# Performance work log

Hardware: AMD Instinct MI355X
Metric: run time of the kernel (lower is better)

The kernel has to match this reference:

```python
import jax, jax.numpy as jnp
import numpy as np

T, B, IN, H, OUT = 1024, 128, 6, 1536, 5


def setup_inputs() -> dict:
    key = jax.random.key(0)
    ks = jax.random.split(key, 11)
    s = 1.0 / np.sqrt(H)  # PyTorch cell init range
    u = lambda k, shape: jax.random.uniform(k, shape, jnp.float32, -s, s)
    return {
        "rnn_input": jax.random.normal(ks[0], (T, B, IN), jnp.float32),
        "W_ih0": u(ks[1], (4 * H, IN)),
        "W_hh0": u(ks[2], (4 * H, H)),
        "b_ih0": u(ks[3], (4 * H,)),
        "b_hh0": u(ks[4], (4 * H,)),
        "W_ih1": u(ks[5], (4 * H, H)),
        "W_hh1": u(ks[6], (4 * H, H)),
        "b_ih1": u(ks[7], (4 * H,)),
        "b_hh1": u(ks[8], (4 * H,)),
        "W_lin": u(ks[9], (OUT, H)),
        "b_lin": u(ks[10], (OUT,)),
    }


def _lstm_cell(x, h, c, W_ih, W_hh, b):
    # PyTorch LSTMCell: gates ordered (input, forget, cell, output)
    gates = x @ W_ih.T + h @ W_hh.T + b  # [B, 4H]
    i, f, g, o = jnp.split(gates, 4, axis=-1)
    c_new = jax.nn.sigmoid(f) * c + jax.nn.sigmoid(i) * jnp.tanh(g)
    h_new = jax.nn.sigmoid(o) * jnp.tanh(c_new)
    return h_new, c_new


def reference(rnn_input, W_ih0, W_hh0, b_ih0, b_hh0,
              W_ih1, W_hh1, b_ih1, b_hh1, W_lin, b_lin):
    b0 = b_ih0 + b_hh0
    b1 = b_ih1 + b_hh1
    batch = rnn_input.shape[1]
    h = rnn_input.dtype
    z = jnp.zeros((batch, H), h)

    def step(carry, x_t):
        h0, c0, h1, c1 = carry
        h0, c0 = _lstm_cell(x_t, h0, c0, W_ih0, W_hh0, b0)
        h1, c1 = _lstm_cell(h0, h1, c1, W_ih1, W_hh1, b1)
        return (h0, c0, h1, c1), None

    (h0, c0, h1, c1), _ = jax.lax.scan(step, (z, z, z, z), rnn_input)
    # Module's forward returns only the last-timestep linear output
    return h1 @ W_lin.T + b_lin  # [B, OUT]
```

## Files before the change

kernel.cpp:

```cpp
#include <hip/hip_runtime.h>

#define TSTEPS 1024
#define BATCH  128
#define HDIM   1536
#define NB_L0  96
#define NB_L1  128
#define NBLK   (NB_L0 + NB_L1)
#define K0P    1600
#define K1P    3072

typedef _Float16 f16x8 __attribute__((ext_vector_type(8)));
typedef float    f32x4 __attribute__((ext_vector_type(4)));

#define OFF_C0   0ul
#define OFF_C1   1024ul
#define OFF_H0   4096ul
#define OFF_H1   (OFF_H0 + 4ul*BATCH*HDIM*2)
#define OFF_WP0  (OFF_H1 + 2ul*BATCH*HDIM*2)
#define OFF_WP1  (OFF_WP0 + 96ul*64*K0P*2)
#define OFF_WLP  (OFF_WP1 + 128ul*48*K1P*2)
#define WS_NEED  (OFF_WLP + 16ul*HDIM*2)

#define SM_PARK  98304
#define SM_CST   147456
#define SM_BG    155648
#define SM_BYTES 155904

#define MFMA(a,b,c) __builtin_amdgcn_mfma_f32_16x16x32_f16(a,b,c,0,0,0)
#define LDSBAR()  asm volatile("s_waitcnt lgkmcnt(0)\n\ts_barrier" ::: "memory")
#define WAITVM8() asm volatile("s_waitcnt vmcnt(8)" ::: "memory")
#define WAITVM0() asm volatile("s_waitcnt vmcnt(0)" ::: "memory")

__device__ __forceinline__ float sgf(float x) { return 1.f/(1.f + __expf(-x)); }
__device__ __forceinline__ float thf(float x) { float e = __expf(2.f*x); return 1.f - 2.f/(e+1.f); }

__device__ __forceinline__ void gld16(const _Float16* g, char* lds) {
  __builtin_amdgcn_global_load_lds(
      (const __attribute__((address_space(1))) unsigned int*)g,
      (__attribute__((address_space(3))) unsigned int*)lds, 16, 0, 0);
}

__device__ __forceinline__ void group_bar(unsigned* lines, unsigned target, int tid) {
  __syncthreads();
  if (tid == 0)
    __hip_atomic_fetch_add(lines + (blockIdx.x & 7)*32, 1u,
                           __ATOMIC_RELEASE, __HIP_MEMORY_SCOPE_AGENT);
  if (tid < 8) {
    while (__hip_atomic_load(lines + tid*32, __ATOMIC_RELAXED,
                             __HIP_MEMORY_SCOPE_AGENT) < target)
      __builtin_amdgcn_s_sleep(1);
    __builtin_amdgcn_fence(__ATOMIC_ACQUIRE, "agent");
  }
  __syncthreads();
}

__device__ __forceinline__ void wait_group(unsigned* lines, unsigned target, int tid) {
  if (tid < 8) {
    while (__hip_atomic_load(lines + tid*32, __ATOMIC_RELAXED,
                             __HIP_MEMORY_SCOPE_AGENT) < target)
      __builtin_amdgcn_s_sleep(1);
    __builtin_amdgcn_fence(__ATOMIC_ACQUIRE, "agent");
  }
  __syncthreads();
}

__global__ void convert_weights(const float* __restrict__ Wih0, const float* __restrict__ Whh0,
                                const float* __restrict__ Wih1, const float* __restrict__ Whh1,
                                const float* __restrict__ Wlin,
                                _Float16* __restrict__ Wp0, _Float16* __restrict__ Wp1,
                                _Float16* __restrict__ Wlp) {
  const unsigned N0 = 96u*64u*K0P, N1 = 128u*48u*K1P, N2 = 16u*HDIM;
  const unsigned NT = N0 + N1 + N2;
  for (unsigned i = blockIdx.x*blockDim.x + threadIdx.x; i < NT; i += gridDim.x*blockDim.x) {
    if (i < N0) {
      unsigned blk = i / (64u*K0P), r = i - blk*64u*K0P;
      unsigned p = r / K0P, kk = r - p*K0P;
      unsigned srow = (p>>4)*HDIM + blk*16 + (p&15);
      float v;
      if (kk < 64u) v = (kk < 6u) ? Wih0[srow*6 + kk] : 0.f;
      else          v = Whh0[(size_t)srow*HDIM + (kk-64u)];
      Wp0[i] = (_Float16)v;
    } else if (i < N0 + N1) {
      unsigned ii = i - N0;
      unsigned blk = ii / (48u*K1P), r = ii - blk*48u*K1P;
      unsigned p = r / K1P, kk = r - p*K1P;
      unsigned srow = (p/12u)*HDIM + blk*12 + (p%12u);
      float v = (kk < (unsigned)HDIM) ? Wih1[(size_t)srow*HDIM + kk]
                                      : Whh1[(size_t)srow*HDIM + (kk-HDIM)];
      Wp1[ii] = (_Float16)v;
    } else {
      unsigned ii = i - N0 - N1;
      unsigned rr = ii / HDIM, k = ii - rr*HDIM;
      Wlp[ii] = (_Float16)(rr < 5 ? Wlin[rr*HDIM + k] : 0.f);
    }
  }
}

__global__ __launch_bounds__(256, 1) void lstm_persistent(
    const float* __restrict__ xall,
    const float* __restrict__ bih0, const float* __restrict__ bhh0,
    const float* __restrict__ bih1, const float* __restrict__ bhh1,
    const float* __restrict__ blin,
    const _Float16* __restrict__ Wp0, const _Float16* __restrict__ Wp1,
    const _Float16* __restrict__ Wlp,
    _Float16* __restrict__ h0b, _Float16* __restrict__ h1b,
    unsigned* __restrict__ c0l, unsigned* __restrict__ c1l,
    float* __restrict__ out)
{
  extern __shared__ __align__(16) char smem[];
  char*  park = smem + SM_PARK;
  float* cst  = (float*)(smem + SM_CST);
  float* bg   = (float*)(smem + SM_BG);
  float* gbuf = (float*)smem;

  const int tid = threadIdx.x, bid = blockIdx.x;
  const int wv = tid >> 6, lane = tid & 63, q = lane >> 4, l15 = lane & 15;
  const int BH = BATCH*HDIM;

  int dmaoff[8];
#pragma unroll
  for (int i = 0; i < 8; ++i) {
    int m = wv*32 + i*4 + (lane>>4), w16 = lane & 15;
    int u = (w16 & 8) | ((w16 ^ (m & 7)) & 7);
    dmaoff[i] = m*HDIM + u*8;
  }
  const int uA = wv*4 + q;
  int addrA[8];
#pragma unroll
  for (int mt = 0; mt < 8; ++mt) {
    int m = mt*16 + l15;
    int swz = (uA & 8) | ((uA ^ (m & 7)) & 7);
    addrA[mt] = m*256 + swz*16;
  }

  if (bid < NB_L0) {
    for (int p = tid; p < 64; p += 256) {
      int srow = (p>>4)*HDIM + (bid<<4) + (p&15);
      bg[p] = bih0[srow] + bhh0[srow];
    }
    for (int i = tid; i < BATCH*16; i += 256) cst[i] = 0.f;
    f16x8 bw[13][4];
#pragma unroll
    for (int wi = 0; wi < 13; ++wi)
#pragma unroll
      for (int nt = 0; nt < 4; ++nt)
        bw[wi][nt] = *(const f16x8*)(Wp0 + ((size_t)(bid*64 + nt*16 + l15))*K0P
                                         + (4*wi + wv)*32 + q*8);
    __syncthreads();

#pragma unroll 1
    for (int s = 0; s < TSTEPS; ++s) {
      if (s >= 4) wait_group(c1l, 16u*(unsigned)(s-3), tid);

      const _Float16* h0r = h0b + (size_t)((s+3)&3)*BH;
      _Float16*       h0w = h0b + (size_t)(s&3)*BH;
      const float*    xs  = xall + (size_t)s*BATCH*6;

#pragma unroll
      for (int i = 0; i < 8; ++i)
        gld16(h0r + 64 + dmaoff[i], smem + 32768 + (wv*8+i)*1024);
#pragma unroll
      for (int i = 0; i < 4; ++i) {
        int sidx = i*256 + tid, m = sidx>>3, w8 = sidx&7;
        int u = w8 ^ (m & 7);
        f16x8 v = {0,0,0,0,0,0,0,0};
        if (u == 0) {
#pragma unroll
          for (int j = 0; j < 6; ++j) v[j] = (_Float16)xs[m*6 + j];
        }
        *(f16x8*)(smem + m*256 + w8*16) = v;
      }
#pragma unroll
      for (int i = 0; i < 4; ++i) {
        int sidx = i*256 + tid, m = sidx>>3, w8 = sidx&7;
        int u8 = (w8 ^ (m & 7)) & 7;
        f16x8 hv = *(const f16x8*)(h0r + m*HDIM + u8*8);
        *(f16x8*)(smem + m*256 + (8 + w8)*16) = hv;
      }
      f32x4 acc[8][4];
#pragma unroll
      for (int mt = 0; mt < 8; ++mt)
#pragma unroll
        for (int nt = 0; nt < 4; ++nt) { f32x4 z = {0,0,0,0}; acc[mt][nt] = z; }

#pragma unroll
      for (int wi = 0; wi < 13; ++wi) {
        if (wi == 12)      WAITVM0();
        else if (wi >= 1)  WAITVM8();
        LDSBAR();
        if (wi + 2 < 13) {
          const _Float16* src = h0r + (wi+2)*128 - 64;
          char* dst = smem + ((wi+2)%3)*32768;
#pragma unroll
          for (int i = 0; i < 8; ++i) gld16(src + dmaoff[i], dst + (wv*8+i)*1024);
        }
        if (4*wi + wv < 50) {
          const char* bs = smem + (wi%3)*32768;
#pragma unroll
          for (int mt = 0; mt < 8; ++mt) {
            f16x8 a = *(const f16x8*)(bs + addrA[mt]);
#pragma unroll
            for (int nt = 0; nt < 4; ++nt)
              acc[mt][nt] = MFMA(a, bw[wi][nt], acc[mt][nt]);
          }
        }
      }
      LDSBAR();

#pragma unroll
      for (int r = 0; r < 4; ++r) {
        int nt = (wv + r) & 3;
#pragma unroll
        for (int mt = 0; mt < 8; ++mt) {
          f32x4 av = (nt==0)?acc[mt][0]:(nt==1)?acc[mt][1]:(nt==2)?acc[mt][2]:acc[mt][3];
          float* p = gbuf + (nt*16 + l15)*132 + (mt*16 + q*4);
          if (r == 0) *(f32x4*)p = av;
          else        { f32x4 o = *(const f32x4*)p; *(f32x4*)p = o + av; }
        }
        LDSBAR();
      }
#pragma unroll
      for (int e = 0; e < 8; ++e) {
        int idx = e*256 + tid, m = idx>>4, j = idx&15;
        float gi = gbuf[j*132 + m]        + bg[j];
        float gf = gbuf[(16+j)*132 + m]   + bg[16+j];
        float gg = gbuf[(32+j)*132 + m]   + bg[32+j];
        float go = gbuf[(48+j)*132 + m]   + bg[48+j];
        float co = cst[m*16 + j];
        float cn = sgf(gf)*co + sgf(gi)*thf(gg);
        cst[m*16 + j] = cn;
        h0w[(size_t)m*HDIM + (bid<<4) + j] = (_Float16)(sgf(go)*thf(cn));
      }
      group_bar(c0l, 12u*(unsigned)(s+1), tid);
    }
  } else {
    const int bid1 = bid - NB_L0;
    for (int p = tid; p < 48; p += 256) {
      int srow = (p/12)*HDIM + bid1*12 + (p%12);
      bg[p] = bih1[srow] + bhh1[srow];
    }
    for (int i = tid; i < 64*12; i += 256) cst[i] = 0.f;
    f16x8 bw1[20][3];
#pragma unroll
    for (int wi = 0; wi < 20; ++wi)
#pragma unroll
      for (int nt = 0; nt < 3; ++nt)
        bw1[wi][nt] = *(const f16x8*)(Wp1 + ((size_t)(bid1*48 + nt*16 + l15))*K1P
                                          + (4*wi + wv)*32 + q*8);
    for (int idx = tid; idx < 16*3*64; idx += 256) {
      int cl = idx/192, rem = idx - cl*192, nt = rem>>6, l = rem&63;
      f16x8 v = *(const f16x8*)(Wp1 + ((size_t)(bid1*48 + nt*16 + (l&15)))*K1P
                                    + (80 + cl)*32 + (l>>4)*8);
      *(f16x8*)(park + idx*16) = v;
    }
    __syncthreads();

#pragma unroll 1
    for (int s = 1; s <= TSTEPS; ++s) {
      wait_group(c0l, 12u*(unsigned)s, tid);

      const _Float16* h0r = h0b + (size_t)((s-1)&3)*BH;
      const _Float16* h1r = h1b + (size_t)(s&1)*BH;
      _Float16*       h1w = h1b + (size_t)((s-1)&1)*BH;

#pragma unroll
      for (int i = 0; i < 8; ++i) gld16(h0r +   0 + dmaoff[i], smem +     0 + (wv*8+i)*1024);
#pragma unroll
      for (int i = 0; i < 8; ++i) gld16(h0r + 128 + dmaoff[i], smem + 32768 + (wv*8+i)*1024);
      f32x4 acc[8][3];
#pragma unroll
      for (int mt = 0; mt < 8; ++mt)
#pragma unroll
        for (int nt = 0; nt < 3; ++nt) { f32x4 z = {0,0,0,0}; acc[mt][nt] = z; }

#pragma unroll
      for (int wi = 0; wi < 24; ++wi) {
        if (wi == 23) WAITVM0(); else WAITVM8();
        LDSBAR();
        if (wi + 2 < 24) {
          int wn = wi + 2;
          const _Float16* src = (wn < 12) ? (h0r + wn*128) : (h1r + (wn-12)*128);
          char* dst = smem + (wn%3)*32768;
#pragma unroll
          for (int i = 0; i < 8; ++i) gld16(src + dmaoff[i], dst + (wv*8+i)*1024);
        }
        const char* bs = smem + (wi%3)*32768;
        if (wi < 20) {
#pragma unroll
          for (int mt = 0; mt < 8; ++mt) {
            f16x8 a = *(const f16x8*)(bs + addrA[mt]);
#pragma unroll
            for (int nt = 0; nt < 3; ++nt)
              acc[mt][nt] = MFMA(a, bw1[wi][nt], acc[mt][nt]);
          }
        } else {
          f16x8 p0 = *(const f16x8*)(park + ((((wi-20)*4 + wv)*3 + 0)*64 + lane)*16);
          f16x8 p1 = *(const f16x8*)(park + ((((wi-20)*4 + wv)*3 + 1)*64 + lane)*16);
          f16x8 p2 = *(const f16x8*)(park + ((((wi-20)*4 + wv)*3 + 2)*64 + lane)*16);
#pragma unroll
          for (int mt = 0; mt < 8; ++mt) {
            f16x8 a = *(const f16x8*)(bs + addrA[mt]);
            acc[mt][0] = MFMA(a, p0, acc[mt][0]);
            acc[mt][1] = MFMA(a, p1, acc[mt][1]);
            acc[mt][2] = MFMA(a, p2, acc[mt][2]);
          }
        }
      }
      LDSBAR();

#pragma unroll
      for (int r = 0; r < 4; ++r) {
        int nt = (wv + r) & 3;
        if (nt < 3) {
#pragma unroll
          for (int mt = 0; mt < 8; ++mt) {
            f32x4 av = (nt==0)?acc[mt][0]:(nt==1)?acc[mt][1]:acc[mt][2];
            float* p = gbuf + (nt*16 + l15)*132 + (mt*16 + q*4);
            if (r == 0) *(f32x4*)p = av;
            else        { f32x4 o = *(const f32x4*)p; *(f32x4*)p = o + av; }
          }
        }
        LDSBAR();
      }
#pragma unroll
      for (int e = 0; e < 8; ++e) {
        int idx = e*256 + tid, m = idx>>4, j = idx&15;
        if (j < 12) {
          float gi = gbuf[j*132 + m]        + bg[j];
          float gf = gbuf[(12+j)*132 + m]   + bg[12+j];
          float gg = gbuf[(24+j)*132 + m]   + bg[24+j];
          float go = gbuf[(36+j)*132 + m]   + bg[36+j];
          float co = cst[m*12 + j];
          float cn = sgf(gf)*co + sgf(gi)*thf(gg);
          cst[m*12 + j] = cn;
          h1w[(size_t)m*HDIM + bid1*12 + j] = (_Float16)(sgf(go)*thf(cn));
        }
      }
      group_bar(c1l, 16u*(unsigned)s, tid);
    }

    if (bid == NB_L0) {
      const _Float16* h1r = h1b + (size_t)((TSTEPS-1)&1)*BH;
      f32x4 a8[8];
#pragma unroll
      for (int i = 0; i < 8; ++i) { f32x4 z = {0,0,0,0}; a8[i] = z; }
      for (int c = wv*12; c < wv*12 + 12; ++c) {
        f16x8 bf = *(const f16x8*)(Wlp + (size_t)l15*HDIM + c*32 + q*8);
#pragma unroll
        for (int mt = 0; mt < 8; ++mt) {
          f16x8 a = *(const f16x8*)(h1r + (size_t)(mt*16 + l15)*HDIM + c*32 + q*8);
          a8[mt] = MFMA(a, bf, a8[mt]);
        }
      }
      float* pl = (float*)smem;
#pragma unroll
      for (int mt = 0; mt < 8; ++mt)
#pragma unroll
        for (int rg = 0; rg < 4; ++rg)
          pl[wv*2048 + (mt*16 + q*4 + rg)*16 + l15] = a8[mt][rg];
      __syncthreads();
      for (int e = tid; e < 640; e += 256) {
        int b = e/5, o = e - 5*b;
        out[e] = blin[o] + pl[b*16+o] + pl[2048 + b*16+o] + pl[4096 + b*16+o] + pl[6144 + b*16+o];
      }
    }
  }
}

extern "C" void kernel_launch(void* const* d_in, const int* in_sizes, int n_in,
                              void* d_out, int out_size, void* d_ws, size_t ws_size,
                              hipStream_t stream) {
  (void)in_sizes; (void)n_in; (void)out_size;
  if (ws_size < WS_NEED) return;

  const float* x    = (const float*)d_in[0];
  const float* Wih0 = (const float*)d_in[1];
  const float* Whh0 = (const float*)d_in[2];
  const float* bih0 = (const float*)d_in[3];
  const float* bhh0 = (const float*)d_in[4];
  const float* Wih1 = (const float*)d_in[5];
  const float* Whh1 = (const float*)d_in[6];
  const float* bih1 = (const float*)d_in[7];
  const float* bhh1 = (const float*)d_in[8];
  const float* Wlin = (const float*)d_in[9];
  const float* blin = (const float*)d_in[10];

  char* ws = (char*)d_ws;
  unsigned*  c0l = (unsigned*)(ws + OFF_C0);
  unsigned*  c1l = (unsigned*)(ws + OFF_C1);
  _Float16*  h0b = (_Float16*)(ws + OFF_H0);
  _Float16*  h1b = (_Float16*)(ws + OFF_H1);
  _Float16*  Wp0 = (_Float16*)(ws + OFF_WP0);
  _Float16*  Wp1 = (_Float16*)(ws + OFF_WP1);
  _Float16*  Wlp = (_Float16*)(ws + OFF_WLP);
  float*     out = (float*)d_out;

  hipMemsetAsync(ws, 0, OFF_WP0, stream);
  hipLaunchKernelGGL(convert_weights, dim3(4096), dim3(256), 0, stream,
                     Wih0, Whh0, Wih1, Whh1, Wlin, Wp0, Wp1, Wlp);

  hipFuncSetAttribute((const void*)lstm_persistent,
                      hipFuncAttributeMaxDynamicSharedMemorySize, 160*1024);

  void* args[14];
  args[0]  = (void*)&x;    args[1]  = (void*)&bih0; args[2]  = (void*)&bhh0;
  args[3]  = (void*)&bih1; args[4]  = (void*)&bhh1; args[5]  = (void*)&blin;
  args[6]  = (void*)&Wp0;  args[7]  = (void*)&Wp1;  args[8]  = (void*)&Wlp;
  args[9]  = (void*)&h0b;  args[10] = (void*)&h1b;  args[11] = (void*)&c0l;
  args[12] = (void*)&c1l;  args[13] = (void*)&out;
  hipError_t err = hipLaunchCooperativeKernel((const void*)lstm_persistent,
                                              dim3(NBLK), dim3(256),
                                              args, (unsigned)SM_BYTES, stream);
  if (err != hipSuccess) {
    hipLaunchKernelGGL(lstm_persistent, dim3(NBLK), dim3(256), SM_BYTES, stream,
                       x, bih0, bhh0, bih1, bhh1, blin, Wp0, Wp1, Wlp,
                       h0b, h1b, c0l, c1l, out);
  }
}
```

Baseline: 28.05 ms.

## Split layer-1 group barrier and prefetch next h0 during gate epilogue

Layer-1 blocks stop doing a full group barrier at the end of each step. They now post an arrival counter and wait for the other layer-1 blocks only right before they first read h1 (at chunk 10), so the h0 part of the matmul overlaps the straggler wait. The next step's h0 wait and DMA prefetch are issued before the gate reduction and epilogue. The gate buffer is moved to a separate LDS region so the prefetch does not clobber it. This adds buffer-reuse hazards, since the h1 double buffer now relies on the split arrive/wait, and the state init now covers the full batch.

```diff
diff --git a/kernel.cpp b/kernel.cpp
--- a/kernel.cpp
+++ b/kernel.cpp
@@ -235,11 +235,12 @@
     }
   } else {
     const int bid1 = bid - NB_L0;
+    float* gbuf1 = (float*)(smem + 65536);
     for (int p = tid; p < 48; p += 256) {
       int srow = (p/12)*HDIM + bid1*12 + (p%12);
       bg[p] = bih1[srow] + bhh1[srow];
     }
-    for (int i = tid; i < 64*12; i += 256) cst[i] = 0.f;
+    for (int i = tid; i < BATCH*12; i += 256) cst[i] = 0.f;
     f16x8 bw1[20][3];
 #pragma unroll
     for (int wi = 0; wi < 20; ++wi)
@@ -255,18 +256,21 @@
     }
     __syncthreads();
 
+    wait_group(c0l, 12u, tid);
+    {
+      const _Float16* h0r1 = h0b;
+#pragma unroll
+      for (int i = 0; i < 8; ++i) gld16(h0r1 +   0 + dmaoff[i], smem +     0 + (wv*8+i)*1024);
+#pragma unroll
+      for (int i = 0; i < 8; ++i) gld16(h0r1 + 128 + dmaoff[i], smem + 32768 + (wv*8+i)*1024);
+    }
+
 #pragma unroll 1
     for (int s = 1; s <= TSTEPS; ++s) {
-      wait_group(c0l, 12u*(unsigned)s, tid);
-
       const _Float16* h0r = h0b + (size_t)((s-1)&3)*BH;
       const _Float16* h1r = h1b + (size_t)(s&1)*BH;
       _Float16*       h1w = h1b + (size_t)((s-1)&1)*BH;
 
-#pragma unroll
-      for (int i = 0; i < 8; ++i) gld16(h0r +   0 + dmaoff[i], smem +     0 + (wv*8+i)*1024);
-#pragma unroll
-      for (int i = 0; i < 8; ++i) gld16(h0r + 128 + dmaoff[i], smem + 32768 + (wv*8+i)*1024);
       f32x4 acc[8][3];
 #pragma unroll
       for (int mt = 0; mt < 8; ++mt)
@@ -275,6 +279,13 @@
 
 #pragma unroll
       for (int wi = 0; wi < 24; ++wi) {
+        if (wi == 10) {
+          const unsigned tgt = 16u*(unsigned)(s-1);
+          while (__hip_atomic_load(c1l + (tid&7)*32, __ATOMIC_RELAXED,
+                                   __HIP_MEMORY_SCOPE_AGENT) < tgt)
+            __builtin_amdgcn_s_sleep(1);
+          asm volatile("s_barrier" ::: "memory");
+        }
         if (wi == 23) WAITVM0(); else WAITVM8();
         LDSBAR();
         if (wi + 2 < 24) {
@@ -294,9 +305,10 @@
               acc[mt][nt] = MFMA(a, bw1[wi][nt], acc[mt][nt]);
           }
         } else {
-          f16x8 p0 = *(const f16x8*)(park + ((((wi-20)*4 + wv)*3 + 0)*64 + lane)*16);
-          f16x8 p1 = *(const f16x8*)(park + ((((wi-20)*4 + wv)*3 + 1)*64 + lane)*16);
-          f16x8 p2 = *(const f16x8*)(park + ((((wi-20)*4 + wv)*3 + 2)*64 + lane)*16);
+          const int cl = (wi-20)*4 + wv;
+          f16x8 p0 = *(const f16x8*)(park + ((cl*3+0)*64 + lane)*16);
+          f16x8 p1 = *(const f16x8*)(park + ((cl*3+1)*64 + lane)*16);
+          f16x8 p2 = *(const f16x8*)(park + ((cl*3+2)*64 + lane)*16);
 #pragma unroll
           for (int mt = 0; mt < 8; ++mt) {
             f16x8 a = *(const f16x8*)(bs + addrA[mt]);
@@ -308,6 +320,15 @@
       }
       LDSBAR();
 
+      if (s < TSTEPS) {
+        wait_group(c0l, 12u*(unsigned)(s+1), tid);
+        const _Float16* h0n = h0b + (size_t)(s&3)*BH;
+#pragma unroll
+        for (int i = 0; i < 8; ++i) gld16(h0n +   0 + dmaoff[i], smem +     0 + (wv*8+i)*1024);
+#pragma unroll
+        for (int i = 0; i < 8; ++i) gld16(h0n + 128 + dmaoff[i], smem + 32768 + (wv*8+i)*1024);
+      }
+
 #pragma unroll
       for (int r = 0; r < 4; ++r) {
         int nt = (wv + r) & 3;
@@ -315,7 +336,7 @@
 #pragma unroll
           for (int mt = 0; mt < 8; ++mt) {
             f32x4 av = (nt==0)?acc[mt][0]:(nt==1)?acc[mt][1]:acc[mt][2];
-            float* p = gbuf + (nt*16 + l15)*132 + (mt*16 + q*4);
+            float* p = gbuf1 + (nt*16 + l15)*132 + (mt*16 + q*4);
             if (r == 0) *(f32x4*)p = av;
             else        { f32x4 o = *(const f32x4*)p; *(f32x4*)p = o + av; }
           }
@@ -326,18 +347,23 @@
       for (int e = 0; e < 8; ++e) {
         int idx = e*256 + tid, m = idx>>4, j = idx&15;
         if (j < 12) {
-          float gi = gbuf[j*132 + m]        + bg[j];
-          float gf = gbuf[(12+j)*132 + m]   + bg[12+j];
-          float gg = gbuf[(24+j)*132 + m]   + bg[24+j];
-          float go = gbuf[(36+j)*132 + m]   + bg[36+j];
+          float gi = gbuf1[j*132 + m]        + bg[j];
+          float gf = gbuf1[(12+j)*132 + m]   + bg[12+j];
+          float gg = gbuf1[(24+j)*132 + m]   + bg[24+j];
+          float go = gbuf1[(36+j)*132 + m]   + bg[36+j];
           float co = cst[m*12 + j];
           float cn = sgf(gf)*co + sgf(gi)*thf(gg);
           cst[m*12 + j] = cn;
           h1w[(size_t)m*HDIM + bid1*12 + j] = (_Float16)(sgf(go)*thf(cn));
         }
       }
-      group_bar(c1l, 16u*(unsigned)s, tid);
-    }
+      __syncthreads();
+      if (tid == 0)
+        __hip_atomic_fetch_add(c1l + (bid & 7)*32, 1u,
+                               __ATOMIC_RELEASE, __HIP_MEMORY_SCOPE_AGENT);
+    }
+
+    wait_group(c1l, 16u*(unsigned)TSTEPS, tid);
 
     if (bid == NB_L0) {
       const _Float16* h1r = h1b + (size_t)((TSTEPS-1)&1)*BH;
```

Result: faster. 27.18 ms (-3.1%).
